# Performance work log

Measured on AMD Instinct MI355X. Metric: run time of the kernel, lower is better.

## Reference

```python
import jax, jax.numpy as jnp
import numpy as np

N = 100000
E = 1600000
IN_C, HID, OUT_C = 128, 256, 32
EPS = 1e-5
NEG_SLOPE = 0.1


def _leaky(x):
    return jnp.where(x >= 0, x, NEG_SLOPE * x)


def _gcn_conv(x, src, dst, ew, W, b, n):
    # x: [n, Fin] -> [n, Fout]; PyG GCNConv: add self-loops (weight 1),
    # symmetric normalization D^-1/2 (A+I) D^-1/2, then linear + bias.
    h = x @ W                                   # [n, Fout]
    loop = jnp.arange(n)
    src_f = jnp.concatenate([src, loop])        # [E+n]
    dst_f = jnp.concatenate([dst, loop])
    ew_f = jnp.concatenate([ew, jnp.ones((n,), x.dtype)])
    deg = jax.ops.segment_sum(ew_f, dst_f, num_segments=n)
    dinv = jnp.where(deg > 0, jax.lax.rsqrt(jnp.maximum(deg, EPS * 0 + 1e-12)), 0.0)
    norm = dinv[src_f] * ew_f * dinv[dst_f]     # [E+n]
    msg = h[src_f] * norm[:, None]              # gather + scale, [E+n, Fout]
    out = jax.ops.segment_sum(msg, dst_f, num_segments=n)
    return out + b


def _bn(x, gamma, beta):
    # training-mode BatchNorm1d over the node dimension
    m = x.mean(axis=0)
    v = x.var(axis=0)
    return (x - m) * jax.lax.rsqrt(v + EPS) * gamma + beta


def setup_inputs() -> dict:
    key = jax.random.key(0)
    ks = jax.random.split(key, 12)
    x = jax.random.normal(ks[0], (N, IN_C), dtype=jnp.float32)
    edge_index = jax.random.randint(ks[1], (2, E), 0, N, dtype=jnp.int64)
    edge_weight = jax.random.uniform(ks[2], (E,), dtype=jnp.float32)

    def lin(k, fi, fo):
        s = 1.0 / np.sqrt(fi)
        k1, k2 = jax.random.split(k)
        W = jax.random.uniform(k1, (fi, fo), jnp.float32, -s, s)
        b = jax.random.uniform(k2, (fo,), jnp.float32, -s, s)
        return W, b

    W1, b1 = lin(ks[3], IN_C, HID)
    W2, b2 = lin(ks[4], HID, HID)
    W3, b3 = lin(ks[5], HID, HID)
    Wl1, bl1 = lin(ks[6], HID, HID)
    Wl2, bl2 = lin(ks[7], HID, OUT_C)
    ones = jnp.ones((HID,), jnp.float32)
    zeros = jnp.zeros((HID,), jnp.float32)
    return {
        "x": x, "edge_index": edge_index, "edge_weight": edge_weight,
        "W1": W1, "b1": b1, "g1": ones, "be1": zeros,
        "W2": W2, "b2": b2, "g2": ones, "be2": zeros,
        "W3": W3, "b3": b3, "g3": ones, "be3": zeros,
        "Wl1": Wl1, "bl1": bl1, "Wl2": Wl2, "bl2": bl2,
    }


def reference(x, edge_index, edge_weight,
              W1, b1, g1, be1,
              W2, b2, g2, be2,
              W3, b3, g3, be3,
              Wl1, bl1, Wl2, bl2):
    src, dst = edge_index[0], edge_index[1]
    h = _gcn_conv(x, src, dst, edge_weight, W1, b1, N)
    h = _leaky(_bn(h, g1, be1))  # dropout = identity (eval)
    h = _gcn_conv(h, src, dst, edge_weight, W2, b2, N)
    h = _leaky(_bn(h, g2, be2))
    h = _gcn_conv(h, src, dst, edge_weight, W3, b3, N)
    h = _leaky(_bn(h, g3, be3))
    h = _leaky(h @ Wl1 + bl1)
    return h @ Wl2 + bl2
```

## Files before the change

### kernel.cpp

```cpp
#include <hip/hip_runtime.h>

#define NN 100000
#define NE 1600000
#define EPS_BN 1e-5f
#define NSHADOW 64
#define STATS_SC_OFF (NSHADOW*512)
#define STATS_SH_OFF (NSHADOW*512 + 256)

typedef unsigned short ushort_t;
typedef unsigned long long u64;
typedef _Float16 f16;
typedef short v8s __attribute__((ext_vector_type(8)));
typedef ushort_t us8 __attribute__((ext_vector_type(8)));
typedef float v4f __attribute__((ext_vector_type(4)));
typedef f16 f16x2 __attribute__((ext_vector_type(2)));
typedef f16 f16x4 __attribute__((ext_vector_type(4)));

__device__ __forceinline__ float lk(float x){ return x >= 0.f ? x : 0.1f*x; }

__device__ __forceinline__ ushort_t f2bf(float x){
  unsigned u = __float_as_uint(x);
  unsigned r = (u + 0x7fffu + ((u >> 16) & 1u)) >> 16;
  return (ushort_t)r;
}
__device__ __forceinline__ float bf2f(ushort_t h){
  return __uint_as_float(((unsigned)h) << 16);
}
__device__ __forceinline__ void split2(float x, ushort_t& hi, ushort_t& lo){
  hi = f2bf(x);
  lo = f2bf(x - bf2f(hi));
}

__device__ __forceinline__ void gload16(const ushort_t* g, ushort_t* l){
  __builtin_amdgcn_global_load_lds((const __attribute__((address_space(1))) void*)g,
                                   (__attribute__((address_space(3))) void*)l, 16, 0, 0);
}

__global__ void zero_acc(u64* __restrict__ acc, int n){
  int i = blockIdx.x*256 + threadIdx.x;
  if (i < n) acc[i] = 0ull;
}

__global__ void edge_hist(const int* __restrict__ dst, const float* __restrict__ ew,
                          u64* __restrict__ acc, ushort_t* __restrict__ rank, int e){
  int i = blockIdx.x*256 + threadIdx.x;
  if (i < e){
    int d = dst[i];
    unsigned fx = (unsigned)(ew[i] * 67108864.0f + 0.5f);
    u64 old = atomicAdd(&acc[d], (1ull << 40) | (u64)fx);
    rank[i] = (ushort_t)(old >> 40);
  }
}

__global__ void finalize_acc(const u64* __restrict__ acc, float* __restrict__ dinv,
                             int* __restrict__ cnt, int n){
  int i = blockIdx.x*256 + threadIdx.x;
  if (i < n){
    u64 v = acc[i];
    cnt[i] = (int)(v >> 40);
    double w = (double)(v & 0xFFFFFFFFFFull) * (1.0/67108864.0);
    dinv[i] = rsqrtf((float)(1.0 + w));
  }
}

__global__ __launch_bounds__(1024) void scan_block(const int* __restrict__ in, int* __restrict__ out,
                                                   int* __restrict__ bsum, int n){
  __shared__ int s[1024];
  int t = threadIdx.x;
  int i = blockIdx.x*1024 + t;
  int v = (i < n) ? in[i] : 0;
  s[t] = v; __syncthreads();
  for (int off = 1; off < 1024; off <<= 1){
    int x = (t >= off) ? s[t-off] : 0;
    __syncthreads();
    s[t] += x;
    __syncthreads();
  }
  if (i < n) out[i] = s[t] - v;
  if (t == 1023) bsum[blockIdx.x] = s[1023];
}

__global__ void scan_small(int* __restrict__ bsum, int nb){
  __shared__ int s[128];
  int t = threadIdx.x;
  int v = (t < nb) ? bsum[t] : 0;
  s[t] = v; __syncthreads();
  for (int off = 1; off < 128; off <<= 1){
    int x = (t >= off) ? s[t-off] : 0;
    __syncthreads();
    s[t] += x;
    __syncthreads();
  }
  if (t < nb) bsum[t] = s[t] - v;
}

__global__ __launch_bounds__(1024) void scan_add(int* __restrict__ rp,
                                                 const int* __restrict__ bsum, int n, int etot){
  int i = blockIdx.x*1024 + threadIdx.x;
  if (i < n) rp[i] += bsum[blockIdx.x];
  if (i == 0) rp[n] = etot;
}

__global__ void fill_csr_k(const int* __restrict__ src, const int* __restrict__ dst,
                           const float* __restrict__ ew, const float* __restrict__ dinv,
                           const int* __restrict__ rp, const ushort_t* __restrict__ rank,
                           int2* __restrict__ csr_sw, int e){
  int i = blockIdx.x*256 + threadIdx.x;
  if (i >= e) return;
  int s = src[i], d = dst[i];
  int pos = rp[d] + (int)rank[i];
  float w = dinv[s] * ew[i] * dinv[d];
  csr_sw[pos] = make_int2(s, __float_as_int(w));
}

__global__ void cvt_x(const float* __restrict__ in, f16* __restrict__ out, int n4){
  int i = blockIdx.x*256 + threadIdx.x;
  if (i >= n4) return;
  float4 v = ((const float4*)in)[i];
  f16x4 h = (f16x4){(f16)v.x, (f16)v.y, (f16)v.z, (f16)v.w};
  ((f16x4*)out)[i] = h;
}

__global__ __launch_bounds__(256) void spmm16(const f16* __restrict__ h,
    const int* __restrict__ rp, const int2* __restrict__ csr_sw,
    const float* __restrict__ dinv, const float* __restrict__ bias,
    float* __restrict__ out, float* __restrict__ stats, int n){
  const int pass = blockIdx.y;
  int nbase = __builtin_amdgcn_readfirstlane(blockIdx.x*16 + (threadIdx.x >> 6)*4);
  if (nbase >= n) return;
  int lane = threadIdx.x & 63;
  const f16* hb = h + pass*128 + lane*2;

  int P[5];
#pragma unroll
  for (int i = 0; i < 5; ++i) P[i] = __builtin_amdgcn_readfirstlane(rp[nbase+i]);
  int nchE[4];
#pragma unroll
  for (int jj = 0; jj < 4; ++jj){
    int nc = (P[jj+1] - P[jj] + 7) >> 3;
    nc = (nc + 1) & ~1;
    nchE[jj] = nc < 2 ? 2 : nc;
  }
  float di0 = dinv[nbase+0], di1 = dinv[nbase+1], di2 = dinv[nbase+2], di3 = dinv[nbase+3];
  f16x2 hv0 = *(const f16x2*)(hb + (size_t)(nbase+0)*256);
  f16x2 hv1 = *(const f16x2*)(hb + (size_t)(nbase+1)*256);
  f16x2 hv2 = *(const f16x2*)(hb + (size_t)(nbase+2)*256);
  f16x2 hv3 = *(const f16x2*)(hb + (size_t)(nbase+3)*256);
  float2 bb = *(const float2*)(bias + pass*128 + lane*2);

  float wA[8], wB[8];
  f16x2 vA[8], vB[8];
  float ax0, ay0, ax1, ay1;
  float ssx = 0.f, ssy = 0.f;
  float sqx = 0.f, sqy = 0.f;

#define LOADCH(W, V, BASE, PEND) do { \
    int2 _e[8]; \
    int _b = (BASE); int _pe = (PEND); \
    _Pragma("unroll") \
    for (int _i = 0; _i < 8; ++_i){ \
      int _pc = _b + _i; \
      _pc = _pc < _pe-1 ? _pc : _pe-1; \
      _pc = _pc > 0 ? _pc : 0; \
      _e[_i] = csr_sw[_pc]; \
    } \
    _Pragma("unroll") \
    for (int _i = 0; _i < 8; ++_i){ \
      W[_i] = (_b + _i < _pe) ? __int_as_float(_e[_i].y) : 0.f; \
      V[_i] = *(const f16x2*)(hb + (size_t)_e[_i].x*256); \
    } \
  } while(0)

#define FMACH(W, V) do { \
    _Pragma("unroll") \
    for (int _i = 0; _i < 8; _i += 2){ \
      ax0 = fmaf(W[_i],   (float)V[_i][0],   ax0); \
      ay0 = fmaf(W[_i],   (float)V[_i][1],   ay0); \
      ax1 = fmaf(W[_i+1], (float)V[_i+1][0], ax1); \
      ay1 = fmaf(W[_i+1], (float)V[_i+1][1], ay1); \
    } \
  } while(0)

#define NODE(jj, DI, HV, PRE) do { \
    const int p0_ = P[jj], pend_ = P[(jj)+1]; \
    const int ncE_ = nchE[jj]; \
    float c0_ = (DI)*(DI); \
    ax0 = fmaf(c0_, (float)(HV)[0], bb.x); \
    ay0 = fmaf(c0_, (float)(HV)[1], bb.y); \
    ax1 = 0.f; ay1 = 0.f; \
    int base_ = p0_ + 8; \
    for (int k_ = 0; k_ + 2 < ncE_; k_ += 2){ \
      LOADCH(wB, vB, base_, pend_); base_ += 8; \
      FMACH(wA, vA); \
      LOADCH(wA, vA, base_, pend_); base_ += 8; \
      FMACH(wB, vB); \
    } \
    LOADCH(wB, vB, base_, pend_); \
    FMACH(wA, vA); \
    PRE; \
    FMACH(wB, vB); \
    { \
      float fx_ = ax0+ax1, fy_ = ay0+ay1; \
      *(float2*)(out + (size_t)(nbase+(jj))*256 + pass*128 + lane*2) = \
          make_float2(fx_, fy_); \
      ssx += fx_; sqx = fmaf(fx_, fx_, sqx); \
      ssy += fy_; sqy = fmaf(fy_, fy_, sqy); \
    } \
  } while(0)

  LOADCH(wA, vA, P[0], P[1]);
  NODE(0, di0, hv0, LOADCH(wA, vA, P[1], P[2]));
  NODE(1, di1, hv1, LOADCH(wA, vA, P[2], P[3]));
  NODE(2, di2, hv2, LOADCH(wA, vA, P[3], P[4]));
  NODE(3, di3, hv3, (void)0);
#undef LOADCH
#undef FMACH
#undef NODE

  __shared__ float red[4][64][4];
  int wid = threadIdx.x >> 6;
  red[wid][lane][0] = ssx; red[wid][lane][1] = ssy;
  red[wid][lane][2] = sqx; red[wid][lane][3] = sqy;
  __syncthreads();
  int c = threadIdx.x;
  if (c < 128){
    float s = 0.f, s2 = 0.f;
#pragma unroll
    for (int w = 0; w < 4; ++w){
      s  += red[w][c>>1][c&1];
      s2 += red[w][c>>1][2 + (c&1)];
    }
    int sh = blockIdx.x & (NSHADOW-1);
    atomicAdd(&stats[sh*512 + pass*128 + c], s);
    atomicAdd(&stats[sh*512 + 256 + pass*128 + c], s2);
  }
}

__global__ __launch_bounds__(256) void spmm_x16(const f16* __restrict__ h,
    const int* __restrict__ rp, const int2* __restrict__ csr_sw,
    const float* __restrict__ dinv,
    ushort_t* __restrict__ ohi, ushort_t* __restrict__ olo, int n){
  int nbase = __builtin_amdgcn_readfirstlane(blockIdx.x*16 + (threadIdx.x >> 6)*4);
  if (nbase >= n) return;
  int lane = threadIdx.x & 63;
  const f16* hb = h + lane*2;

  int P[5];
#pragma unroll
  for (int i = 0; i < 5; ++i) P[i] = __builtin_amdgcn_readfirstlane(rp[nbase+i]);
  int nchE[4];
#pragma unroll
  for (int jj = 0; jj < 4; ++jj){
    int nc = (P[jj+1] - P[jj] + 7) >> 3;
    nc = (nc + 1) & ~1;
    nchE[jj] = nc < 2 ? 2 : nc;
  }
  float di0 = dinv[nbase+0], di1 = dinv[nbase+1], di2 = dinv[nbase+2], di3 = dinv[nbase+3];
  f16x2 hv0 = *(const f16x2*)(hb + (size_t)(nbase+0)*128);
  f16x2 hv1 = *(const f16x2*)(hb + (size_t)(nbase+1)*128);
  f16x2 hv2 = *(const f16x2*)(hb + (size_t)(nbase+2)*128);
  f16x2 hv3 = *(const f16x2*)(hb + (size_t)(nbase+3)*128);

  float wA[8], wB[8];
  f16x2 vA[8], vB[8];
  float ax0, ay0, ax1, ay1;

#define LOADCH(W, V, BASE, PEND) do { \
    int2 _e[8]; \
    int _b = (BASE); int _pe = (PEND); \
    _Pragma("unroll") \
    for (int _i = 0; _i < 8; ++_i){ \
      int _pc = _b + _i; \
      _pc = _pc < _pe-1 ? _pc : _pe-1; \
      _pc = _pc > 0 ? _pc : 0; \
      _e[_i] = csr_sw[_pc]; \
    } \
    _Pragma("unroll") \
    for (int _i = 0; _i < 8; ++_i){ \
      W[_i] = (_b + _i < _pe) ? __int_as_float(_e[_i].y) : 0.f; \
      V[_i] = *(const f16x2*)(hb + (size_t)_e[_i].x*128); \
    } \
  } while(0)

#define FMACH(W, V) do { \
    _Pragma("unroll") \
    for (int _i = 0; _i < 8; _i += 2){ \
      ax0 = fmaf(W[_i],   (float)V[_i][0],   ax0); \
      ay0 = fmaf(W[_i],   (float)V[_i][1],   ay0); \
      ax1 = fmaf(W[_i+1], (float)V[_i+1][0], ax1); \
      ay1 = fmaf(W[_i+1], (float)V[_i+1][1], ay1); \
    } \
  } while(0)

#define NODE(jj, DI, HV, PRE) do { \
    const int p0_ = P[jj], pend_ = P[(jj)+1]; \
    const int ncE_ = nchE[jj]; \
    float c0_ = (DI)*(DI); \
    ax0 = c0_ * (float)(HV)[0]; \
    ay0 = c0_ * (float)(HV)[1]; \
    ax1 = 0.f; ay1 = 0.f; \
    int base_ = p0_ + 8; \
    for (int k_ = 0; k_ + 2 < ncE_; k_ += 2){ \
      LOADCH(wB, vB, base_, pend_); base_ += 8; \
      FMACH(wA, vA); \
      LOADCH(wA, vA, base_, pend_); base_ += 8; \
      FMACH(wB, vB); \
    } \
    LOADCH(wB, vB, base_, pend_); \
    FMACH(wA, vA); \
    PRE; \
    FMACH(wB, vB); \
    { \
      float ax_ = ax0 + ax1, ay_ = ay0 + ay1; \
      ushort_t hx_, lx_, hy_, ly_; \
      split2(ax_, hx_, lx_); \
      split2(ay_, hy_, ly_); \
      size_t o_ = (size_t)(nbase+(jj))*128 + lane*2; \
      ohi[o_] = hx_; ohi[o_+1] = hy_; \
      olo[o_] = lx_; olo[o_+1] = ly_; \
    } \
  } while(0)

  LOADCH(wA, vA, P[0], P[1]);
  NODE(0, di0, hv0, LOADCH(wA, vA, P[1], P[2]));
  NODE(1, di1, hv1, LOADCH(wA, vA, P[2], P[3]));
  NODE(2, di2, hv2, LOADCH(wA, vA, P[3], P[4]));
  NODE(3, di3, hv3, (void)0);
#undef LOADCH
#undef FMACH
#undef NODE
}

__global__ void zero_stats(float* __restrict__ stats){
  stats[blockIdx.x*256 + threadIdx.x] = 0.f;
}

__global__ void bn_final(float* __restrict__ stats, const float* __restrict__ g,
                         const float* __restrict__ be, int n){
  int c = threadIdx.x;
  float s = 0.f, s2 = 0.f;
  for (int k = 0; k < NSHADOW; ++k){
    s  += stats[k*512 + c];
    s2 += stats[k*512 + 256 + c];
  }
  float inv_n = 1.0f / (float)n;
  float mean = s * inv_n;
  float var  = fmaxf(s2 * inv_n - mean*mean, 0.f);
  float sc   = g[c] * rsqrtf(var + EPS_BN);
  stats[STATS_SC_OFF + c] = sc;
  stats[STATS_SH_OFF + c] = be[c] - mean * sc;
}

__global__ void wsplit(const float* __restrict__ W, ushort_t* __restrict__ hiT,
                       ushort_t* __restrict__ loT, int K, int M){
  int i = blockIdx.x*256 + threadIdx.x;
  if (i >= K*M) return;
  int k = i / M, m = i % M;
  ushort_t h, l;
  split2(W[i], h, l);
  hiT[(size_t)m*K + k] = h;
  loT[(size_t)m*K + k] = l;
}

template<int BM, int BN, int WM, int WN, int ACT, int OMODE, int STATS, int AMODE>
__global__ __launch_bounds__(256) void gemm_mfma(
    const ushort_t* __restrict__ Ahi_g, const ushort_t* __restrict__ Alo_g,
    const float* __restrict__ Af_g,
    const ushort_t* __restrict__ Bhi_g, const ushort_t* __restrict__ Blo_g,
    const float* __restrict__ bias,
    float* __restrict__ Cf, ushort_t* __restrict__ Chi, ushort_t* __restrict__ Clo,
    f16* __restrict__ Ch, float* __restrict__ stats_g,
    int nrows, int K, int M){
  constexpr int FI = WM/16, FJ = WN/16;
  constexpr int WCOLS = BN/WN;
  __shared__ ushort_t sAhi[BM*32];
  __shared__ ushort_t sAlo[BM*32];
  __shared__ ushort_t sBhi[BN*32];
  __shared__ ushort_t sBlo[BN*32];
  __shared__ float sSC[AMODE ? 256 : 1];
  __shared__ float sSH[AMODE ? 256 : 1];
  const int tid  = threadIdx.x;
  const int wave = tid >> 6;
  const int lane = tid & 63;
  const int r0 = blockIdx.x * BM;
  const int c0 = blockIdx.y * BN;
  const int wr0 = (wave / WCOLS) * WM;
  const int wc0 = (wave % WCOLS) * WN;
  const int m = lane & 15, q = lane >> 4;

  if constexpr (AMODE == 1){
    if (tid < K){
      sSC[tid] = stats_g[STATS_SC_OFF + tid];
      sSH[tid] = stats_g[STATS_SH_OFF + tid];
    }
    __syncthreads();
  }

  v4f acc[FI][FJ];
#pragma unroll
  for (int i = 0; i < FI; ++i)
#pragma unroll
    for (int j = 0; j < FJ; ++j) acc[i][j] = (v4f){0.f,0.f,0.f,0.f};

  const int srow = lane >> 2;
  const int kqlog = (lane & 3) ^ ((srow >> 1) & 3);
  const int fsw = (q ^ ((m >> 1) & 3)) * 8;

  for (int kt = 0; kt < K; kt += 32){
    if constexpr (AMODE == 0){
#pragma unroll
      for (int cc = wave; cc < BM/16; cc += 4){
        int gr = r0 + cc*16 + srow;
        gr = min(gr, nrows - 1);
        size_t go = (size_t)gr*K + kt + kqlog*8;
        gload16(Ahi_g + go, &sAhi[cc*512]);
        gload16(Alo_g + go, &sAlo[cc*512]);
      }
    } else {
#pragma unroll
      for (int pidx = tid; pidx < BM*4; pidx += 256){
        int row  = pidx >> 2;
        int kq   = pidx & 3;
        int gr   = min(r0 + row, nrows - 1);
        int ch0  = kt + kq*8;
        const float* ap = Af_g + (size_t)gr*K + ch0;
        float4 a0 = *(const float4*)ap;
        float4 a1 = *(const float4*)(ap + 4);
        float4 sc0 = *(const float4*)&sSC[ch0];
        float4 sc1 = *(const float4*)&sSC[ch0 + 4];
        float4 sh0 = *(const float4*)&sSH[ch0];
        float4 sh1 = *(const float4*)&sSH[ch0 + 4];
        float va[8] = {a0.x, a0.y, a0.z, a0.w, a1.x, a1.y, a1.z, a1.w};
        float vc[8] = {sc0.x, sc0.y, sc0.z, sc0.w, sc1.x, sc1.y, sc1.z, sc1.w};
        float vh[8] = {sh0.x, sh0.y, sh0.z, sh0.w, sh1.x, sh1.y, sh1.z, sh1.w};
        us8 hi8, lo8;
#pragma unroll
        for (int j = 0; j < 8; ++j){
          float v = lk(fmaf(va[j], vc[j], vh[j]));
          ushort_t hh, ll;
          split2(v, hh, ll);
          hi8[j] = hh; lo8[j] = ll;
        }
        int off = row*32 + (kq ^ ((row >> 1) & 3))*8;
        *(us8*)&sAhi[off] = hi8;
        *(us8*)&sAlo[off] = lo8;
      }
    }
    for (int cc = wave; cc < BN/16; cc += 4){
      int gr = c0 + cc*16 + srow;
      size_t go = (size_t)gr*K + kt + kqlog*8;
      gload16(Bhi_g + go, &sBhi[cc*512]);
      gload16(Blo_g + go, &sBlo[cc*512]);
    }
    __syncthreads();

    v8s ah[FI], al[FI], bh[FJ], bl[FJ];
#pragma unroll
    for (int i = 0; i < FI; ++i){
      int off = (wr0 + i*16 + m)*32 + fsw;
      ah[i] = *(const v8s*)&sAhi[off];
      al[i] = *(const v8s*)&sAlo[off];
    }
#pragma unroll
    for (int j = 0; j < FJ; ++j){
      int off = (wc0 + j*16 + m)*32 + fsw;
      bh[j] = *(const v8s*)&sBhi[off];
      bl[j] = *(const v8s*)&sBlo[off];
    }
#pragma unroll
    for (int i = 0; i < FI; ++i)
#pragma unroll
      for (int j = 0; j < FJ; ++j){
        acc[i][j] = __builtin_amdgcn_mfma_f32_16x16x32_bf16(ah[i], bh[j], acc[i][j], 0, 0, 0);
        acc[i][j] = __builtin_amdgcn_mfma_f32_16x16x32_bf16(ah[i], bl[j], acc[i][j], 0, 0, 0);
        acc[i][j] = __builtin_amdgcn_mfma_f32_16x16x32_bf16(al[i], bh[j], acc[i][j], 0, 0, 0);
      }
    __syncthreads();
  }

  __shared__ float cst[STATS ? 2*BN : 1];
  if constexpr (STATS){
    for (int t = tid; t < 2*BN; t += 256) cst[t] = 0.f;
    __syncthreads();
  }
  float stj[FJ], stq[FJ];
#pragma unroll
  for (int j = 0; j < FJ; ++j){ stj[j] = 0.f; stq[j] = 0.f; }

#pragma unroll
  for (int i = 0; i < FI; ++i){
#pragma unroll
    for (int j = 0; j < FJ; ++j){
      int col = c0 + wc0 + j*16 + m;
      float bv = (ACT >= 1) ? bias[col] : 0.f;
#pragma unroll
      for (int r = 0; r < 4; ++r){
        int row = r0 + wr0 + i*16 + q*4 + r;
        if (row >= nrows) continue;
        float v = acc[i][j][r] + bv;
        if (ACT == 1) v = lk(v);
        if constexpr (STATS){
          stj[j] += v;
          stq[j] = fmaf(v, v, stq[j]);
        }
        size_t o = (size_t)row*M + col;
        if (OMODE == 1){
          ushort_t h, l; split2(v, h, l);
          Chi[o] = h; Clo[o] = l;
        } else if (OMODE == 2){
          Ch[o] = (f16)v;
        } else {
          Cf[o] = v;
        }
      }
    }
  }

  if constexpr (STATS){
#pragma unroll
    for (int j = 0; j < FJ; ++j){
      int cl = wc0 + j*16 + m;
      atomicAdd(&cst[cl*2 + 0], stj[j]);
      atomicAdd(&cst[cl*2 + 1], stq[j]);
    }
    __syncthreads();
    for (int t = tid; t < BN; t += 256){
      int sh = (blockIdx.x + blockIdx.y) & (NSHADOW-1);
      atomicAdd(&stats_g[sh*512 + c0 + t],        cst[t*2 + 0]);
      atomicAdd(&stats_g[sh*512 + 256 + c0 + t],  cst[t*2 + 1]);
    }
  }
}

extern "C" void kernel_launch(void* const* d_in, const int* in_sizes, int n_in,
                              void* d_out, int out_size, void* d_ws, size_t ws_size,
                              hipStream_t stream){
  const float* x   = (const float*)d_in[0];
  const int*   ei  = (const int*)  d_in[1];
  const float* ew  = (const float*)d_in[2];
  const float* W1  = (const float*)d_in[3];
  const float* b1  = (const float*)d_in[4];
  const float* g1  = (const float*)d_in[5];
  const float* be1 = (const float*)d_in[6];
  const float* W2  = (const float*)d_in[7];
  const float* b2  = (const float*)d_in[8];
  const float* g2  = (const float*)d_in[9];
  const float* be2 = (const float*)d_in[10];
  const float* W3  = (const float*)d_in[11];
  const float* b3  = (const float*)d_in[12];
  const float* g3  = (const float*)d_in[13];
  const float* be3 = (const float*)d_in[14];
  const float* Wl1 = (const float*)d_in[15];
  const float* bl1 = (const float*)d_in[16];
  const float* Wl2 = (const float*)d_in[17];
  const float* bl2 = (const float*)d_in[18];
  const int* src = ei;
  const int* dst = ei + NE;

  char* p = (char*)d_ws;
  auto carve = [&](size_t bytes)->void*{
    void* r = (void*)p;
    p += (bytes + 255) & ~(size_t)255;
    return r;
  };
  float*    dinv    = (float*)   carve((size_t)NN*4);
  int*      rp      = (int*)     carve((size_t)(NN+1)*4);
  int*      cnt     = (int*)     carve((size_t)NN*4);
  int*      bsum    = (int*)     carve(256*4);
  float*    stats   = (float*)   carve((size_t)(NSHADOW*512 + 512)*4);
  u64*      acc64   = (u64*)     carve((size_t)NN*8);
  int2*     csr_sw  = (int2*)    carve((size_t)NE*8);
  float*    S1      = (float*)   carve((size_t)NN*256*4);
  float*    S2      = (float*)   carve((size_t)NN*256*4);
  ushort_t* W1tH    = (ushort_t*)carve(128*256*2);
  ushort_t* W1tL    = (ushort_t*)carve(128*256*2);
  ushort_t* W2tH    = (ushort_t*)carve(256*256*2);
  ushort_t* W2tL    = (ushort_t*)carve(256*256*2);
  ushort_t* W3tH    = (ushort_t*)carve(256*256*2);
  ushort_t* W3tL    = (ushort_t*)carve(256*256*2);
  ushort_t* Wl1tH   = (ushort_t*)carve(256*256*2);
  ushort_t* Wl1tL   = (ushort_t*)carve(256*256*2);
  ushort_t* Wl2tH   = (ushort_t*)carve(256*32*2);
  ushort_t* Wl2tL   = (ushort_t*)carve(256*32*2);

  ushort_t* S1h256 = (ushort_t*)S1;  ushort_t* S1l256 = S1h256 + (size_t)NN*256;
  ushort_t* S1h128 = (ushort_t*)S1;  ushort_t* S1l128 = S1h128 + (size_t)NN*128;
  ushort_t* rank   = (ushort_t*)S2;
  f16*      x16    = (f16*)S2;
  f16*      H2f16  = (f16*)S1;
  f16*      H3f16  = (f16*)S1;

  const int nb = (NN + 1023) / 1024;
  const dim3 spmm_grid((NN + 15) / 16, 2);
  const int spmm_blocks = (NN + 15) / 16;
  const int gemm_blocks = (NN + 63) / 64;

  zero_acc<<<(NN+255)/256, 256, 0, stream>>>(acc64, NN);
  edge_hist<<<(NE+255)/256, 256, 0, stream>>>(dst, ew, acc64, rank, NE);
  finalize_acc<<<(NN+255)/256, 256, 0, stream>>>(acc64, dinv, cnt, NN);
  scan_block<<<nb, 1024, 0, stream>>>(cnt, rp, bsum, NN);
  scan_small<<<1, 128, 0, stream>>>(bsum, nb);
  scan_add<<<nb, 1024, 0, stream>>>(rp, bsum, NN, NE);
  fill_csr_k<<<(NE+255)/256, 256, 0, stream>>>(src, dst, ew, dinv, rp, rank, csr_sw, NE);

  wsplit<<<(128*256+255)/256, 256, 0, stream>>>(W1,  W1tH,  W1tL,  128, 256);
  wsplit<<<(256*256+255)/256, 256, 0, stream>>>(W2,  W2tH,  W2tL,  256, 256);
  wsplit<<<(256*256+255)/256, 256, 0, stream>>>(W3,  W3tH,  W3tL,  256, 256);
  wsplit<<<(256*256+255)/256, 256, 0, stream>>>(Wl1, Wl1tH, Wl1tL, 256, 256);
  wsplit<<<(256*32 +255)/256, 256, 0, stream>>>(Wl2, Wl2tH, Wl2tL, 256, 32);

  dim3 gridOut((NN+127)/128, 1);

  cvt_x<<<(NN*32+255)/256, 256, 0, stream>>>(x, x16, NN*32);
  spmm_x16<<<spmm_blocks, 256, 0, stream>>>(x16, rp, csr_sw, dinv, S1h128, S1l128, NN);
  zero_stats<<<128, 256, 0, stream>>>(stats);
  gemm_mfma<64,256,64,64,2,0,1,0><<<gemm_blocks, 256, 0, stream>>>(
      S1h128, S1l128, nullptr, W1tH, W1tL, b1, S2, nullptr, nullptr, nullptr, stats, NN, 128, 256);
  bn_final<<<1, 256, 0, stream>>>(stats, g1, be1, NN);

  zero_stats<<<128, 256, 0, stream>>>(stats);
  gemm_mfma<64,256,64,64,0,2,0,1><<<gemm_blocks, 256, 0, stream>>>(
      nullptr, nullptr, S2, W2tH, W2tL, nullptr, nullptr, nullptr, nullptr, H2f16, stats, NN, 256, 256);
  spmm16<<<spmm_grid, 256, 0, stream>>>(H2f16, rp, csr_sw, dinv, b2, S2, stats, NN);
  bn_final<<<1, 256, 0, stream>>>(stats, g2, be2, NN);

  zero_stats<<<128, 256, 0, stream>>>(stats);
  gemm_mfma<64,256,64,64,0,2,0,1><<<gemm_blocks, 256, 0, stream>>>(
      nullptr, nullptr, S2, W3tH, W3tL, nullptr, nullptr, nullptr, nullptr, H3f16, stats, NN, 256, 256);
  spmm16<<<spmm_grid, 256, 0, stream>>>(H3f16, rp, csr_sw, dinv, b3, S2, stats, NN);
  bn_final<<<1, 256, 0, stream>>>(stats, g3, be3, NN);

  gemm_mfma<64,256,64,64,1,1,0,1><<<gemm_blocks, 256, 0, stream>>>(
      nullptr, nullptr, S2, Wl1tH, Wl1tL, bl1, nullptr, S1h256, S1l256, nullptr, stats, NN, 256, 256);
  gemm_mfma<128,32,32,32,2,0,0,0><<<gridOut, 256, 0, stream>>>(
      S1h256, S1l256, nullptr, Wl2tH, Wl2tL, bl2, (float*)d_out, nullptr, nullptr, nullptr, nullptr, NN, 256, 32);
}
```

Before: 919.8 us.

## Fuse the two MLP head GEMMs into one kernel, keeping the hidden tile in LDS

Replaces the Wl1 GEMM (which wrote a bf16 hi/lo split of a 100000x256 intermediate to global memory) and the separate Wl2 GEMM with a single kernel. The first GEMM's leaky-relu output stays in shared memory, reusing the B tile buffers. The second GEMM then runs per 32-row half, with each wave computing a partial K slice and reducing through shared-memory atomics. This removes the large intermediate write and re-read and one launch. In exchange it adds LDS atomics, extra syncs, and Wl2 fragments read directly from global memory.

```diff
diff --git a/kernel.cpp b/kernel.cpp
--- a/kernel.cpp
+++ b/kernel.cpp
@@ -368,8 +368,7 @@
     const float* __restrict__ Af_g,
     const ushort_t* __restrict__ Bhi_g, const ushort_t* __restrict__ Blo_g,
     const float* __restrict__ bias,
-    float* __restrict__ Cf, ushort_t* __restrict__ Chi, ushort_t* __restrict__ Clo,
-    f16* __restrict__ Ch, float* __restrict__ stats_g,
+    float* __restrict__ Cf, f16* __restrict__ Ch, float* __restrict__ stats_g,
     int nrows, int K, int M){
   constexpr int FI = WM/16, FJ = WN/16;
   constexpr int WCOLS = BN/WN;
@@ -504,10 +503,7 @@
           stq[j] = fmaf(v, v, stq[j]);
         }
         size_t o = (size_t)row*M + col;
-        if (OMODE == 1){
-          ushort_t h, l; split2(v, h, l);
-          Chi[o] = h; Clo[o] = l;
-        } else if (OMODE == 2){
+        if (OMODE == 2){
           Ch[o] = (f16)v;
         } else {
           Cf[o] = v;
@@ -529,6 +525,176 @@
       atomicAdd(&stats_g[sh*512 + c0 + t],        cst[t*2 + 0]);
       atomicAdd(&stats_g[sh*512 + 256 + c0 + t],  cst[t*2 + 1]);
     }
+  }
+}
+
+__global__ __launch_bounds__(256) void head_fused(
+    const float* __restrict__ Af_g,
+    const ushort_t* __restrict__ B1h, const ushort_t* __restrict__ B1l,
+    const float* __restrict__ bl1,
+    const ushort_t* __restrict__ B2h, const ushort_t* __restrict__ B2l,
+    const float* __restrict__ bl2,
+    const float* __restrict__ stats_g,
+    float* __restrict__ outp, int nrows){
+  constexpr int BM = 64, BN = 256, K = 256;
+  __shared__ ushort_t sAhi[BM*32];
+  __shared__ ushort_t sAlo[BM*32];
+  __shared__ ushort_t sBhi[BN*32];
+  __shared__ ushort_t sBlo[BN*32];
+  __shared__ float sSC[256];
+  __shared__ float sSH[256];
+  __shared__ float sRed[32*32];
+  const int tid  = threadIdx.x;
+  const int wave = tid >> 6;
+  const int lane = tid & 63;
+  const int r0 = blockIdx.x * BM;
+  const int wc0 = wave * 64;
+  const int m = lane & 15, q = lane >> 4;
+
+  if (tid < K){
+    sSC[tid] = stats_g[STATS_SC_OFF + tid];
+    sSH[tid] = stats_g[STATS_SH_OFF + tid];
+  }
+  __syncthreads();
+
+  v4f acc[4][4];
+#pragma unroll
+  for (int i = 0; i < 4; ++i)
+#pragma unroll
+    for (int j = 0; j < 4; ++j) acc[i][j] = (v4f){0.f,0.f,0.f,0.f};
+
+  const int srow = lane >> 2;
+  const int kqlog = (lane & 3) ^ ((srow >> 1) & 3);
+  const int fsw = (q ^ ((m >> 1) & 3)) * 8;
+
+  for (int kt = 0; kt < K; kt += 32){
+#pragma unroll
+    for (int pidx = tid; pidx < BM*4; pidx += 256){
+      int row  = pidx >> 2;
+      int kq   = pidx & 3;
+      int gr   = min(r0 + row, nrows - 1);
+      int ch0  = kt + kq*8;
+      const float* ap = Af_g + (size_t)gr*K + ch0;
+      float4 a0 = *(const float4*)ap;
+      float4 a1 = *(const float4*)(ap + 4);
+      float4 sc0 = *(const float4*)&sSC[ch0];
+      float4 sc1 = *(const float4*)&sSC[ch0 + 4];
+      float4 sh0 = *(const float4*)&sSH[ch0];
+      float4 sh1 = *(const float4*)&sSH[ch0 + 4];
+      float va[8] = {a0.x, a0.y, a0.z, a0.w, a1.x, a1.y, a1.z, a1.w};
+      float vc[8] = {sc0.x, sc0.y, sc0.z, sc0.w, sc1.x, sc1.y, sc1.z, sc1.w};
+      float vh[8] = {sh0.x, sh0.y, sh0.z, sh0.w, sh1.x, sh1.y, sh1.z, sh1.w};
+      us8 hi8, lo8;
+#pragma unroll
+      for (int j = 0; j < 8; ++j){
+        float v = lk(fmaf(va[j], vc[j], vh[j]));
+        ushort_t hh, ll;
+        split2(v, hh, ll);
+        hi8[j] = hh; lo8[j] = ll;
+      }
+      int off = row*32 + (kq ^ ((row >> 1) & 3))*8;
+      *(us8*)&sAhi[off] = hi8;
+      *(us8*)&sAlo[off] = lo8;
+    }
+    for (int cc = wave; cc < BN/16; cc += 4){
+      int gr = cc*16 + srow;
+      size_t go = (size_t)gr*K + kt + kqlog*8;
+      gload16(B1h + go, &sBhi[cc*512]);
+      gload16(B1l + go, &sBlo[cc*512]);
+    }
+    __syncthreads();
+
+    v8s ah[4], al[4], bh[4], bl[4];
+#pragma unroll
+    for (int i = 0; i < 4; ++i){
+      int off = (i*16 + m)*32 + fsw;
+      ah[i] = *(const v8s*)&sAhi[off];
+      al[i] = *(const v8s*)&sAlo[off];
+    }
+#pragma unroll
+    for (int j = 0; j < 4; ++j){
+      int off = (wc0 + j*16 + m)*32 + fsw;
+      bh[j] = *(const v8s*)&sBhi[off];
+      bl[j] = *(const v8s*)&sBlo[off];
+    }
+#pragma unroll
+    for (int i = 0; i < 4; ++i)
+#pragma unroll
+      for (int j = 0; j < 4; ++j){
+        acc[i][j] = __builtin_amdgcn_mfma_f32_16x16x32_bf16(ah[i], bh[j], acc[i][j], 0, 0, 0);
+        acc[i][j] = __builtin_amdgcn_mfma_f32_16x16x32_bf16(ah[i], bl[j], acc[i][j], 0, 0, 0);
+        acc[i][j] = __builtin_amdgcn_mfma_f32_16x16x32_bf16(al[i], bh[j], acc[i][j], 0, 0, 0);
+      }
+    __syncthreads();
+  }
+
+  float b1c[4];
+#pragma unroll
+  for (int j = 0; j < 4; ++j) b1c[j] = bl1[wc0 + j*16 + m];
+
+#pragma unroll
+  for (int h = 0; h < 2; ++h){
+    sRed[tid] = 0.f; sRed[tid + 256] = 0.f; sRed[tid + 512] = 0.f; sRed[tid + 768] = 0.f;
+#pragma unroll
+    for (int ii = 0; ii < 2; ++ii){
+      int i = 2*h + ii;
+#pragma unroll
+      for (int j = 0; j < 4; ++j){
+        int col = wc0 + j*16 + m;
+        int t2c = col >> 5;
+        int cch = (col >> 3) & 3;
+        int cwi = col & 7;
+#pragma unroll
+        for (int r = 0; r < 4; ++r){
+          int rl = ii*16 + q*4 + r;
+          float v = lk(acc[i][j][r] + b1c[j]);
+          ushort_t hh, ll;
+          split2(v, hh, ll);
+          int off = rl*256 + t2c*32 + (cch ^ ((rl >> 1) & 3))*8 + cwi;
+          sBhi[off] = hh;
+          sBlo[off] = ll;
+        }
+      }
+    }
+    __syncthreads();
+#pragma unroll
+    for (int i2 = 0; i2 < 2; ++i2){
+#pragma unroll
+      for (int j2 = 0; j2 < 2; ++j2){
+        v4f a2 = (v4f){0.f,0.f,0.f,0.f};
+#pragma unroll
+        for (int t2 = 0; t2 < 2; ++t2){
+          int kt2 = wc0 + t2*32;
+          int aoff = (i2*16 + m)*256 + kt2 + fsw;
+          v8s a2h = *(const v8s*)&sBhi[aoff];
+          v8s a2l = *(const v8s*)&sBlo[aoff];
+          size_t boff = (size_t)(j2*16 + m)*256 + kt2 + q*8;
+          v8s b2h = *(const v8s*)&B2h[boff];
+          v8s b2l = *(const v8s*)&B2l[boff];
+          a2 = __builtin_amdgcn_mfma_f32_16x16x32_bf16(a2h, b2h, a2, 0, 0, 0);
+          a2 = __builtin_amdgcn_mfma_f32_16x16x32_bf16(a2h, b2l, a2, 0, 0, 0);
+          a2 = __builtin_amdgcn_mfma_f32_16x16x32_bf16(a2l, b2h, a2, 0, 0, 0);
+        }
+#pragma unroll
+        for (int r = 0; r < 4; ++r)
+          atomicAdd(&sRed[(i2*16 + q*4 + r)*32 + j2*16 + m], a2[r]);
+      }
+    }
+    __syncthreads();
+    {
+      int rl = tid >> 3;
+      int c4 = (tid & 7) * 4;
+      int grow = r0 + h*32 + rl;
+      if (grow < nrows){
+        float4 o;
+        o.x = sRed[rl*32 + c4+0] + bl2[c4+0];
+        o.y = sRed[rl*32 + c4+1] + bl2[c4+1];
+        o.z = sRed[rl*32 + c4+2] + bl2[c4+2];
+        o.w = sRed[rl*32 + c4+3] + bl2[c4+3];
+        *(float4*)(outp + (size_t)grow*32 + c4) = o;
+      }
+    }
+    __syncthreads();
   }
 }
 
@@ -583,7 +749,6 @@
   ushort_t* Wl2tH   = (ushort_t*)carve(256*32*2);
   ushort_t* Wl2tL   = (ushort_t*)carve(256*32*2);
 
-  ushort_t* S1h256 = (ushort_t*)S1;  ushort_t* S1l256 = S1h256 + (size_t)NN*256;
   ushort_t* S1h128 = (ushort_t*)S1;  ushort_t* S1l128 = S1h128 + (size_t)NN*128;
   ushort_t* rank   = (ushort_t*)S2;
   f16*      x16    = (f16*)S2;
@@ -609,29 +774,25 @@
   wsplit<<<(256*256+255)/256, 256, 0, stream>>>(Wl1, Wl1tH, Wl1tL, 256, 256);
   wsplit<<<(256*32 +255)/256, 256, 0, stream>>>(Wl2, Wl2tH, Wl2tL, 256, 32);
 
-  dim3 gridOut((NN+127)/128, 1);
-
   cvt_x<<<(NN*32+255)/256, 256, 0, stream>>>(x, x16, NN*32);
   spmm_x16<<<spmm_blocks, 256, 0, stream>>>(x16, rp, csr_sw, dinv, S1h128, S1l128, NN);
   zero_stats<<<128, 256, 0, stream>>>(stats);
   gemm_mfma<64,256,64,64,2,0,1,0><<<gemm_blocks, 256, 0, stream>>>(
-      S1h128, S1l128, nullptr, W1tH, W1tL, b1, S2, nullptr, nullptr, nullptr, stats, NN, 128, 256);
+      S1h128, S1l128, nullptr, W1tH, W1tL, b1, S2, nullptr, stats, NN, 128, 256);
   bn_final<<<1, 256, 0, stream>>>(stats, g1, be1, NN);
 
   zero_stats<<<128, 256, 0, stream>>>(stats);
   gemm_mfma<64,256,64,64,0,2,0,1><<<gemm_blocks, 256, 0, stream>>>(
-      nullptr, nullptr, S2, W2tH, W2tL, nullptr, nullptr, nullptr, nullptr, H2f16, stats, NN, 256, 256);
+      nullptr, nullptr, S2, W2tH, W2tL, nullptr, nullptr, H2f16, stats, NN, 256, 256);
   spmm16<<<spmm_grid, 256, 0, stream>>>(H2f16, rp, csr_sw, dinv, b2, S2, stats, NN);
   bn_final<<<1, 256, 0, stream>>>(stats, g2, be2, NN);
 
   zero_stats<<<128, 256, 0, stream>>>(stats);
   gemm_mfma<64,256,64,64,0,2,0,1><<<gemm_blocks, 256, 0, stream>>>(
-      nullptr, nullptr, S2, W3tH, W3tL, nullptr, nullptr, nullptr, nullptr, H3f16, stats, NN, 256, 256);
+      nullptr, nullptr, S2, W3tH, W3tL, nullptr, nullptr, H3f16, stats, NN, 256, 256);
   spmm16<<<spmm_grid, 256, 0, stream>>>(H3f16, rp, csr_sw, dinv, b3, S2, stats, NN);
   bn_final<<<1, 256, 0, stream>>>(stats, g3, be3, NN);
 
-  gemm_mfma<64,256,64,64,1,1,0,1><<<gemm_blocks, 256, 0, stream>>>(
-      nullptr, nullptr, S2, Wl1tH, Wl1tL, bl1, nullptr, S1h256, S1l256, nullptr, stats, NN, 256, 256);
-  gemm_mfma<128,32,32,32,2,0,0,0><<<gridOut, 256, 0, stream>>>(
-      S1h256, S1l256, nullptr, Wl2tH, Wl2tL, bl2, (float*)d_out, nullptr, nullptr, nullptr, nullptr, NN, 256, 32);
-}
+  head_fused<<<gemm_blocks, 256, 0, stream>>>(
+      S2, Wl1tH, Wl1tL, bl1, Wl2tH, Wl2tL, bl2, stats, (float*)d_out, NN);
+}
```

Result: slower. 960.8 us (+4.5%).
